# Performance work log

Hardware: AMD Instinct MI355X
Metric: run time of the kernel (lower is better)

Reference implementation:

```python
import jax, jax.numpy as jnp
import numpy as np

DN = ('NCH', 'OIH', 'NCH')

def conv1d(x, w, b, pad):
    y = jax.lax.conv_general_dilated(x, w, (1,), [(pad, pad)], dimension_numbers=DN)
    return y if b is None else y + b[None, :, None]

def bn_eval(x, g, b, m, v, eps):
    s = g * jax.lax.rsqrt(v + eps)
    return x * s[None, :, None] + (b - m * s)[None, :, None]

def swish(x):
    return x * jax.nn.sigmoid(x)

def setup_inputs() -> dict:
    key = jax.random.key(0)
    ks = jax.random.split(key, 8)
    B, T, P = 16, 8192, 32
    inp = {
        'x': jax.random.normal(ks[0], (B, 1, T), jnp.float32),
        'conv_w': jax.random.normal(ks[1], (512, 1, 9), jnp.float32) * 0.1,
        'bn_g': jnp.ones((512,), jnp.float32),
        'bn_b': jnp.zeros((512,), jnp.float32),
        'bn_m': jnp.zeros((512,), jnp.float32),
        'bn_v': jnp.ones((512,), jnp.float32),
        'p1_w': jax.random.normal(ks[2], (P, 2, 31), jnp.float32) * 0.1,
        'p1_b': jnp.zeros((P,), jnp.float32),
        'pbn1_g': jnp.ones((P,), jnp.float32),
        'pbn1_b': jnp.zeros((P,), jnp.float32),
        'pbn1_m': jnp.zeros((P,), jnp.float32),
        'pbn1_v': jnp.ones((P,), jnp.float32),
        'p2_w': jax.random.normal(ks[3], (P, P, 15), jnp.float32) * 0.05,
        'p2_b': jnp.zeros((P,), jnp.float32),
        'pbn2_g': jnp.ones((P,), jnp.float32),
        'pbn2_b': jnp.zeros((P,), jnp.float32),
        'pbn2_m': jnp.zeros((P,), jnp.float32),
        'pbn2_v': jnp.ones((P,), jnp.float32),
        'p3_w': jax.random.normal(ks[4], (2, P, 15), jnp.float32) * 0.001,  # source scales last conv weight by 0.01
        'p3_b': jnp.full((2,), -np.log(2.0), jnp.float32),                 # source sets bias to -log(2)
        'norm_mean': jnp.ones((1,), jnp.float32),                           # eval-mode renorm buffer
    }
    return inp

def reference(x, conv_w, bn_g, bn_b, bn_m, bn_v,
              p1_w, p1_b, pbn1_g, pbn1_b, pbn1_m, pbn1_v,
              p2_w, p2_b, pbn2_g, pbn2_b, pbn2_m, pbn2_v,
              p3_w, p3_b, norm_mean):
    B, _, T = x.shape
    # main conv -> BN(eps=1e-3) -> GLU(dim=1); dropout is identity in eval
    h = conv1d(x, conv_w, None, 9 // 2)                 # [B, 512, T]
    h = bn_eval(h, bn_g, bn_b, bn_m, bn_v, 1e-3)
    a, g = jnp.split(h, 2, axis=1)
    features = a * jax.nn.sigmoid(g)                    # [B, 256, T]
    # predictor on cat([x, x*x])
    j = conv1d(jnp.concatenate([x, x * x], axis=1), p1_w, p1_b, 15)
    j = swish(bn_eval(j, pbn1_g, pbn1_b, pbn1_m, pbn1_v, 1e-5))
    j = conv1d(j, p2_w, p2_b, 7)
    j = swish(bn_eval(j, pbn2_g, pbn2_b, pbn2_m, pbn2_v, 1e-5))
    j = conv1d(j, p3_w, p3_b, 7)                        # [B, 2, T]
    weights = jax.nn.sigmoid(j[:, 0, :])                # [B, T]
    moves = jax.nn.sigmoid(j[:, 1, :])
    bmoves = moves
    moves = moves * norm_mean[0]                        # eval: renorm = norm_mean buffer
    # CIF-style dynamic pooling (row_pool), vectorized over batch
    feats = jnp.transpose(features, (0, 2, 1))          # [B, T, C]
    fw = feats * weights[..., None]
    poses = jnp.cumsum(jax.lax.stop_gradient(moves), axis=1)  # moves.detach() in source
    floors = jnp.floor(poses)
    w1 = 1.0 - (poses - floors)
    w2 = poses - floors
    fl = floors.astype(jnp.int32)
    ce = fl + 1
    Lmax = T + 2  # static bound: poses <= T so ceil index <= T+1
    C = fw.shape[2]
    def pool(fw_i, fl_i, ce_i, w1_i, w2_i):
        out = jnp.zeros((Lmax, C), fw_i.dtype)
        out = out.at[fl_i].add(w1_i[:, None] * fw_i)
        out = out.at[ce_i].add(w2_i[:, None] * fw_i)
        return out
    x_evs = jax.vmap(pool)(fw, fl, ce, w1, w2)          # [B, Lmax, C]
    lens = fl[:, -1] + 2                                 # int(ceils[-1]) + 1
    x_evs = jnp.transpose(x_evs, (0, 2, 1))             # [B, C, Lmax]
    pad = 3 - (Lmax % 3)
    x_evs = jnp.pad(x_evs, ((0, 0), (0, 0), (0, pad)))
    return x_evs, lens, bmoves, weights
```

## Files before the change

kernel.cpp:

```cpp
#include <hip/hip_runtime.h>
#include <math.h>

static constexpr int TT = 8192;
static constexpr int LFULL = 8196;

static constexpr size_t XE_OFF   = 0;
static constexpr size_t LENS_OFF = (size_t)16*256*LFULL;
static constexpr size_t BM_OFF   = LENS_OFF + 16;
static constexpr size_t WT_OFF   = BM_OFF + (size_t)16*TT;

static constexpr size_t U_OFF     = 0;
static constexpr size_t V_OFF     = U_OFF + (size_t)16*32*TT;
static constexpr size_t MOVES_OFF = V_OFF + (size_t)16*32*TT;
static constexpr size_t POSES_OFF = MOVES_OFF + (size_t)16*TT;
static constexpr size_t C1_OFF    = POSES_OFF + (size_t)16*TT;
static constexpr size_t C2_OFF    = C1_OFF + (size_t)16*TT;

__device__ __forceinline__ float sig_(float z) { return 1.0f / (1.0f + __expf(-z)); }

__global__ __launch_bounds__(256) void k_conv1(
    const float* __restrict__ x,
    const float* __restrict__ p1w, const float* __restrict__ p1b,
    const float* __restrict__ g1, const float* __restrict__ b1,
    const float* __restrict__ m1, const float* __restrict__ v1,
    float* __restrict__ u)
{
    __shared__ float xin[2 * 320];
    __shared__ float w1t[2 * 992];
    const int tid = threadIdx.x;
    const int b = blockIdx.y;
    const int t0 = blockIdx.x * 256;

    for (int idx = tid; idx < 640; idx += 256) {
        int ci = idx / 320, xl = idx - ci * 320;
        int id = t0 - 15 + xl;
        float val = 0.f;
        if (xl < 286 && id >= 0 && id < TT) val = x[b * TT + id];
        xin[idx] = ci ? val * val : val;
    }
    for (int idx = tid; idx < 1984; idx += 256) {
        int c = idx / 62; int r = idx - c * 62; int ci = r / 31; int k = r - ci * 31;
        w1t[ci * 992 + c * 31 + k] = p1w[idx];
    }
    __syncthreads();

    const int tg = tid >> 5, c = tid & 31;
    float acc[32];
    const float bias = p1b[c];
#pragma unroll
    for (int i = 0; i < 32; ++i) acc[i] = bias;

    for (int h = 0; h < 4; ++h) {
        for (int ci = 0; ci < 2; ++ci) {
            float win[40];
            const float4* wp = (const float4*)(&xin[ci * 320 + tg * 32 + h * 8]);
#pragma unroll
            for (int r = 0; r < 10; ++r) {
                float4 q = wp[r];
                win[4*r] = q.x; win[4*r+1] = q.y; win[4*r+2] = q.z; win[4*r+3] = q.w;
            }
#pragma unroll
            for (int k = 0; k < 31; ++k) {
                float w = w1t[ci * 992 + c * 31 + k];
#pragma unroll
                for (int i = 0; i < 8; ++i) acc[h*8+i] = fmaf(w, win[i + k], acc[h*8+i]);
            }
        }
    }
    const float s = g1[c] * rsqrtf(v1[c] + 1e-5f);
    const float sh = b1[c] - m1[c] * s;
    float* up = &u[((size_t)(b * 32 + c)) * TT + t0 + tg * 32];
#pragma unroll
    for (int i = 0; i < 8; ++i) {
        float z0 = fmaf(acc[4*i+0], s, sh);
        float z1 = fmaf(acc[4*i+1], s, sh);
        float z2 = fmaf(acc[4*i+2], s, sh);
        float z3 = fmaf(acc[4*i+3], s, sh);
        ((float4*)up)[i] = make_float4(z0 * sig_(z0), z1 * sig_(z1), z2 * sig_(z2), z3 * sig_(z3));
    }
}

__global__ __launch_bounds__(256) void k_conv2(
    const float* __restrict__ u,
    const float* __restrict__ p2w, const float* __restrict__ p2b,
    const float* __restrict__ g2, const float* __restrict__ b2,
    const float* __restrict__ m2, const float* __restrict__ v2,
    float* __restrict__ vout)
{
    __shared__ float uld[32 * 144];
    __shared__ float w2t[32 * 240];
    const int tid = threadIdx.x;
    const int b = blockIdx.y;
    const int t0 = blockIdx.x * 128;
    const int ch = blockIdx.z;

    for (int idx = tid; idx < 32 * 144; idx += 256) {
        int ci = idx / 144, tl = idx - ci * 144;
        int tg = t0 - 7 + tl;
        float val = 0.f;
        if (tl < 142 && tg >= 0 && tg < TT) val = u[((size_t)(b * 32 + ci)) * TT + tg];
        uld[idx] = val;
    }
    for (int idx = tid; idx < 32 * 240; idx += 256) {
        int ci = idx / 240; int r = idx - ci * 240; int cl = r / 15; int k = r - cl * 15;
        w2t[idx] = p2w[(ch * 16 + cl) * 480 + ci * 15 + k];
    }
    __syncthreads();

    const int tg = tid >> 4, cl = tid & 15;
    const int c = ch * 16 + cl;
    float acc[8];
    const float bias = p2b[c];
#pragma unroll
    for (int i = 0; i < 8; ++i) acc[i] = bias;

    for (int ci = 0; ci < 32; ++ci) {
        float win[24];
        const float4* wp = (const float4*)(&uld[ci * 144 + tg * 8]);
#pragma unroll
        for (int r = 0; r < 6; ++r) {
            float4 q = wp[r];
            win[4*r] = q.x; win[4*r+1] = q.y; win[4*r+2] = q.z; win[4*r+3] = q.w;
        }
#pragma unroll
        for (int k = 0; k < 15; ++k) {
            float w = w2t[ci * 240 + cl * 15 + k];
#pragma unroll
            for (int i = 0; i < 8; ++i) acc[i] = fmaf(w, win[i + k], acc[i]);
        }
    }
    const float s = g2[c] * rsqrtf(v2[c] + 1e-5f);
    const float sh = b2[c] - m2[c] * s;
    float o[8];
#pragma unroll
    for (int i = 0; i < 8; ++i) { float z = fmaf(acc[i], s, sh); o[i] = z * sig_(z); }
    float* vp = &vout[((size_t)(b * 32 + c)) * TT + t0 + tg * 8];
    ((float4*)vp)[0] = make_float4(o[0], o[1], o[2], o[3]);
    ((float4*)vp)[1] = make_float4(o[4], o[5], o[6], o[7]);
}

__global__ __launch_bounds__(256) void k_conv3(
    const float* __restrict__ vin,
    const float* __restrict__ p3w, const float* __restrict__ p3b,
    const float* __restrict__ nm,
    float* __restrict__ outw, float* __restrict__ outbm, float* __restrict__ moves)
{
    __shared__ float vld[32 * 272];
    const int tid = threadIdx.x;
    const int b = blockIdx.y;
    const int t0 = blockIdx.x * 256;

    for (int idx = tid; idx < 32 * 272; idx += 256) {
        int ci = idx / 272, tl = idx - ci * 272;
        int tg = t0 - 7 + tl;
        float val = 0.f;
        if (tl < 270 && tg >= 0 && tg < TT) val = vin[((size_t)(b * 32 + ci)) * TT + tg];
        vld[idx] = val;
    }
    __syncthreads();

    float a0 = p3b[0], a1 = p3b[1];
    for (int ci = 0; ci < 32; ++ci) {
        float win[15];
#pragma unroll
        for (int k = 0; k < 15; ++k) win[k] = vld[ci * 272 + tid + k];
#pragma unroll
        for (int k = 0; k < 15; ++k) {
            a0 = fmaf(p3w[ci * 15 + k], win[k], a0);
            a1 = fmaf(p3w[480 + ci * 15 + k], win[k], a1);
        }
    }
    const int t = t0 + tid;
    const float wt = sig_(a0);
    const float bm = sig_(a1);
    outw[b * TT + t] = wt;
    outbm[b * TT + t] = bm;
    moves[b * TT + t] = bm * nm[0];
}

__global__ __launch_bounds__(1024) void k_scan(
    const float* __restrict__ moves, const float* __restrict__ wts,
    float* __restrict__ poses, float* __restrict__ coef1, float* __restrict__ coef2,
    float* __restrict__ lens)
{
    __shared__ float wsum[16];
    const int tid = threadIdx.x;
    const int b = blockIdx.x;
    const int lane = tid & 63, wv = tid >> 6;
    float carry = 0.f;

    const float4* mv4 = (const float4*)&moves[b * TT];
    const float4* wt4 = (const float4*)&wts[b * TT];
    float4* po4 = (float4*)&poses[b * TT];
    float4* c14 = (float4*)&coef1[b * TT];
    float4* c24 = (float4*)&coef2[b * TT];

    for (int chunk = 0; chunk < 2; ++chunk) {
        const int idx = chunk * 1024 + tid;
        float4 m = mv4[idx];
        const float s = m.x + m.y + m.z + m.w;
        float v = s;
#pragma unroll
        for (int off = 1; off < 64; off <<= 1) {
            float n = __shfl_up(v, off, 64);
            if (lane >= off) v += n;
        }
        if (lane == 63) wsum[wv] = v;
        __syncthreads();
        float pre = carry;
        for (int w = 0; w < wv; ++w) pre += wsum[w];
        float tot = 0.f;
#pragma unroll
        for (int w = 0; w < 16; ++w) tot += wsum[w];
        const float base = pre + (v - s);
        const float p0 = base + m.x;
        const float p1 = p0 + m.y;
        const float p2 = p1 + m.z;
        const float p3 = p2 + m.w;
        po4[idx] = make_float4(p0, p1, p2, p3);
        const float4 w4 = wt4[idx];
        const float fr0 = p0 - floorf(p0), fr1 = p1 - floorf(p1);
        const float fr2 = p2 - floorf(p2), fr3 = p3 - floorf(p3);
        c14[idx] = make_float4((1.f - fr0) * w4.x, (1.f - fr1) * w4.y,
                               (1.f - fr2) * w4.z, (1.f - fr3) * w4.w);
        c24[idx] = make_float4(fr0 * w4.x, fr1 * w4.y, fr2 * w4.z, fr3 * w4.w);
        if (chunk == 1 && tid == 1023) lens[b] = floorf(p3) + 2.0f;
        carry += tot;
        __syncthreads();
    }
}

static constexpr int LTILE = 32;
static constexpr int CHK = 256;

__global__ __launch_bounds__(256) void k_pool(
    const float* __restrict__ x,
    const float* __restrict__ cw,
    const float* __restrict__ bng, const float* __restrict__ bnb,
    const float* __restrict__ bnm, const float* __restrict__ bnv,
    const float* __restrict__ poses, const float* __restrict__ coef1, const float* __restrict__ coef2,
    float* __restrict__ xevs)
{
    __shared__ float out_lds[256 * 33];
    __shared__ float4 xl4[68];
    __shared__ float4 c1l4[CHK / 4], c2l4[CHK / 4];
    __shared__ int lbs[LTILE + 2];
    float* xl = (float*)xl4;
    float* c1l = (float*)c1l4;
    float* c2l = (float*)c2l4;

    const int tid = threadIdx.x;
    const int b = blockIdx.y;
    const int l0 = blockIdx.x * LTILE;
    const int LTa = min(LTILE, LFULL - l0);

    if (tid < LTa + 2) {
        const float lf = (float)(l0 - 1 + tid);
        int lo = 0, hi = TT;
        const float* pp = &poses[b * TT];
        while (lo < hi) { int mid = (lo + hi) >> 1; if (pp[mid] >= lf) hi = mid; else lo = mid + 1; }
        lbs[tid] = lo;
    }
    __syncthreads();

    const int t_lo = lbs[0];
    const int t_hi = lbs[LTa + 1];
    const size_t rowbase = (size_t)b * 256 * LFULL + l0;

    if (t_lo >= t_hi) {
        const float4 z = make_float4(0.f, 0.f, 0.f, 0.f);
#pragma unroll
        for (int it = 0; it < 8; ++it) {
            int idx4 = it * 256 + tid;
            int cc = idx4 >> 3, q = (idx4 & 7) << 2;
            if (l0 + q < LFULL)
                *(float4*)(&xevs[rowbase + (size_t)cc * LFULL + q]) = z;
        }
        return;
    }

    {
        float4 z = make_float4(0.f, 0.f, 0.f, 0.f);
        float4* oz = (float4*)out_lds;
        for (int idx = tid; idx < (256 * 33) / 4; idx += 256) oz[idx] = z;
    }

    const int c = tid;
    float wa[9], wg[9];
#pragma unroll
    for (int k = 0; k < 9; ++k) { wa[k] = cw[c * 9 + k]; wg[k] = cw[(c + 256) * 9 + k]; }
    const float sa = bng[c] * rsqrtf(bnv[c] + 1e-3f);
    const float sha = bnb[c] - bnm[c] * sa;
    const float sg = bng[c + 256] * rsqrtf(bnv[c + 256] + 1e-3f);
    const float shg = bnb[c + 256] - bnm[c + 256] * sg;

    const float* xg = &x[b * TT];
    const float* c1g = &coef1[b * TT];
    const float* c2g = &coef2[b * TT];

    float accA = 0.f, accB = 0.f;
    int j = 0;
    int nb = lbs[1];

    for (int cs = t_lo; cs < t_hi; cs += CHK) {
        const int ce = min(cs + CHK, t_hi);
        const int len = ce - cs;
        __syncthreads();
        for (int idx = tid; idx < len + 12; idx += 256) {
            int id = cs - 4 + idx;
            xl[idx] = (id >= 0 && id < TT) ? xg[id] : 0.f;
        }
        if (tid < len) { c1l[tid] = c1g[cs + tid]; c2l[tid] = c2g[cs + tid]; }
        __syncthreads();

        const int len4 = len >> 2;
        for (int g = 0; g < len4; ++g) {
            float4 A = xl4[g], Bq = xl4[g + 1], Cq = xl4[g + 2];
            float w[12] = {A.x, A.y, A.z, A.w, Bq.x, Bq.y, Bq.z, Bq.w, Cq.x, Cq.y, Cq.z, Cq.w};
            float f[4];
#pragma unroll
            for (int i = 0; i < 4; ++i) {
                float s0 = 0.f, s1 = 0.f;
#pragma unroll
                for (int k = 0; k < 9; ++k) { s0 = fmaf(wa[k], w[i + k], s0); s1 = fmaf(wg[k], w[i + k], s1); }
                const float av = fmaf(s0, sa, sha);
                const float gv = fmaf(s1, sg, shg);
                f[i] = av * sig_(gv);
            }
            float4 c1v = c1l4[g], c2v = c2l4[g];
            const float c1a[4] = {c1v.x, c1v.y, c1v.z, c1v.w};
            const float c2a[4] = {c2v.x, c2v.y, c2v.z, c2v.w};
            const int tb = cs + (g << 2);
#pragma unroll
            for (int i = 0; i < 4; ++i) {
                const int t = tb + i;
                while (t >= nb) {
                    int li = j - 1;
                    if (li >= 0 && li < LTa) out_lds[c * 33 + li] = accA;
                    accA = accB; accB = 0.f;
                    ++j;
                    nb = lbs[j + 1];
                }
                accA = fmaf(c1a[i], f[i], accA);
                accB = fmaf(c2a[i], f[i], accB);
            }
        }
        for (int t = cs + (len4 << 2); t < ce; ++t) {
            const int il = t - cs;
            float s0 = 0.f, s1 = 0.f;
#pragma unroll
            for (int k = 0; k < 9; ++k) { float xv = xl[il + k]; s0 = fmaf(wa[k], xv, s0); s1 = fmaf(wg[k], xv, s1); }
            const float av = fmaf(s0, sa, sha);
            const float gv = fmaf(s1, sg, shg);
            const float f0 = av * sig_(gv);
            while (t >= nb) {
                int li = j - 1;
                if (li >= 0 && li < LTa) out_lds[c * 33 + li] = accA;
                accA = accB; accB = 0.f;
                ++j;
                nb = lbs[j + 1];
            }
            accA = fmaf(c1l[il], f0, accA);
            accB = fmaf(c2l[il], f0, accB);
        }
    }
    {
        int li = j - 1;
        if (li >= 0 && li < LTa) out_lds[c * 33 + li] = accA;
    }
    __syncthreads();

#pragma unroll
    for (int it = 0; it < 8; ++it) {
        int idx4 = it * 256 + tid;
        int cc = idx4 >> 3, q = (idx4 & 7) << 2;
        if (l0 + q < LFULL) {
            float4 o;
            o.x = out_lds[cc * 33 + q + 0];
            o.y = out_lds[cc * 33 + q + 1];
            o.z = out_lds[cc * 33 + q + 2];
            o.w = out_lds[cc * 33 + q + 3];
            *(float4*)(&xevs[rowbase + (size_t)cc * LFULL + q]) = o;
        }
    }
}

extern "C" void kernel_launch(void* const* d_in, const int* in_sizes, int n_in,
                              void* d_out, int out_size, void* d_ws, size_t ws_size,
                              hipStream_t stream) {
    (void)in_sizes; (void)n_in; (void)out_size; (void)ws_size;
    const float* x      = (const float*)d_in[0];
    const float* conv_w = (const float*)d_in[1];
    const float* bn_g   = (const float*)d_in[2];
    const float* bn_b   = (const float*)d_in[3];
    const float* bn_m   = (const float*)d_in[4];
    const float* bn_v   = (const float*)d_in[5];
    const float* p1_w   = (const float*)d_in[6];
    const float* p1_b   = (const float*)d_in[7];
    const float* pbn1_g = (const float*)d_in[8];
    const float* pbn1_b = (const float*)d_in[9];
    const float* pbn1_m = (const float*)d_in[10];
    const float* pbn1_v = (const float*)d_in[11];
    const float* p2_w   = (const float*)d_in[12];
    const float* p2_b   = (const float*)d_in[13];
    const float* pbn2_g = (const float*)d_in[14];
    const float* pbn2_b = (const float*)d_in[15];
    const float* pbn2_m = (const float*)d_in[16];
    const float* pbn2_v = (const float*)d_in[17];
    const float* p3_w   = (const float*)d_in[18];
    const float* p3_b   = (const float*)d_in[19];
    const float* nm     = (const float*)d_in[20];

    float* out = (float*)d_out;
    float* ws  = (float*)d_ws;
    float* u     = ws + U_OFF;
    float* v     = ws + V_OFF;
    float* moves = ws + MOVES_OFF;
    float* poses = ws + POSES_OFF;
    float* coef1 = ws + C1_OFF;
    float* coef2 = ws + C2_OFF;
    float* xevs  = out + XE_OFF;
    float* lens  = out + LENS_OFF;
    float* bmv   = out + BM_OFF;
    float* wts   = out + WT_OFF;

    k_conv1<<<dim3(32, 16), 256, 0, stream>>>(x, p1_w, p1_b, pbn1_g, pbn1_b, pbn1_m, pbn1_v, u);
    k_conv2<<<dim3(64, 16, 2), 256, 0, stream>>>(u, p2_w, p2_b, pbn2_g, pbn2_b, pbn2_m, pbn2_v, v);
    k_conv3<<<dim3(32, 16), 256, 0, stream>>>(v, p3_w, p3_b, nm, wts, bmv, moves);
    k_scan<<<16, 1024, 0, stream>>>(moves, wts, poses, coef1, coef2, lens);
    k_pool<<<dim3(257, 16), 256, 0, stream>>>(x, conv_w, bn_g, bn_b, bn_m, bn_v, poses, coef1, coef2, xevs);
}
```

Baseline: 365.7 us.

## Emit segment boundaries from scan and halve pool tile size

The scan kernel now writes, for each output slot, the first input index whose cumulative position reaches it, so the pool kernel reads its boundaries directly instead of binary-searching the poses array. The poses buffer is dropped and the boundary array reuses the start of the workspace already consumed by the earlier conv stages. The pool tile shrinks from 32 to 16 output slots with a smaller chunk, doubling the grid to improve occupancy and load balance, at the cost of recomputing more halo convolution work per block. The boundary fill loop in the scan is serial per thread, so a thread whose positions cross many slot boundaries does extra work.

```diff
diff --git a/kernel.cpp b/kernel.cpp
--- a/kernel.cpp
+++ b/kernel.cpp
@@ -3,6 +3,7 @@
 
 static constexpr int TT = 8192;
 static constexpr int LFULL = 8196;
+static constexpr int BSTRIDE = LFULL + 2;
 
 static constexpr size_t XE_OFF   = 0;
 static constexpr size_t LENS_OFF = (size_t)16*256*LFULL;
@@ -12,9 +13,9 @@
 static constexpr size_t U_OFF     = 0;
 static constexpr size_t V_OFF     = U_OFF + (size_t)16*32*TT;
 static constexpr size_t MOVES_OFF = V_OFF + (size_t)16*32*TT;
-static constexpr size_t POSES_OFF = MOVES_OFF + (size_t)16*TT;
-static constexpr size_t C1_OFF    = POSES_OFF + (size_t)16*TT;
+static constexpr size_t C1_OFF    = MOVES_OFF + (size_t)16*TT;
 static constexpr size_t C2_OFF    = C1_OFF + (size_t)16*TT;
+static constexpr size_t BND_OFF   = U_OFF;
 
 __device__ __forceinline__ float sig_(float z) { return 1.0f / (1.0f + __expf(-z)); }
 
@@ -180,8 +181,8 @@
 
 __global__ __launch_bounds__(1024) void k_scan(
     const float* __restrict__ moves, const float* __restrict__ wts,
-    float* __restrict__ poses, float* __restrict__ coef1, float* __restrict__ coef2,
-    float* __restrict__ lens)
+    float* __restrict__ coef1, float* __restrict__ coef2,
+    int* __restrict__ bnd, float* __restrict__ lens)
 {
     __shared__ float wsum[16];
     const int tid = threadIdx.x;
@@ -189,9 +190,13 @@
     const int lane = tid & 63, wv = tid >> 6;
     float carry = 0.f;
 
+    int* bb = &bnd[b * BSTRIDE];
+    for (int i = tid; i < BSTRIDE; i += 1024) bb[i] = TT;
+    if (tid == 0) { bb[0] = 0; bb[1] = 0; }
+    __syncthreads();
+
     const float4* mv4 = (const float4*)&moves[b * TT];
     const float4* wt4 = (const float4*)&wts[b * TT];
-    float4* po4 = (float4*)&poses[b * TT];
     float4* c14 = (float4*)&coef1[b * TT];
     float4* c24 = (float4*)&coef2[b * TT];
 
@@ -217,32 +222,46 @@
         const float p1 = p0 + m.y;
         const float p2 = p1 + m.z;
         const float p3 = p2 + m.w;
-        po4[idx] = make_float4(p0, p1, p2, p3);
         const float4 w4 = wt4[idx];
         const float fr0 = p0 - floorf(p0), fr1 = p1 - floorf(p1);
         const float fr2 = p2 - floorf(p2), fr3 = p3 - floorf(p3);
         c14[idx] = make_float4((1.f - fr0) * w4.x, (1.f - fr1) * w4.y,
                                (1.f - fr2) * w4.z, (1.f - fr3) * w4.w);
         c24[idx] = make_float4(fr0 * w4.x, fr1 * w4.y, fr2 * w4.z, fr3 * w4.w);
+        {
+            int lf = (int)floorf(base) + 1;
+            const int lfe = (int)floorf(p3);
+            const int tbase = idx << 2;
+            for (; lf <= lfe; ++lf) {
+                const float lff = (float)lf;
+                int t = tbase;
+                if (p0 >= lff) { }
+                else if (p1 >= lff) t += 1;
+                else if (p2 >= lff) t += 2;
+                else t += 3;
+                if (lf + 1 < BSTRIDE) bb[lf + 1] = t;
+            }
+        }
         if (chunk == 1 && tid == 1023) lens[b] = floorf(p3) + 2.0f;
         carry += tot;
         __syncthreads();
     }
 }
 
-static constexpr int LTILE = 32;
-static constexpr int CHK = 256;
+static constexpr int LTILE = 16;
+static constexpr int CHK = 128;
 
 __global__ __launch_bounds__(256) void k_pool(
     const float* __restrict__ x,
     const float* __restrict__ cw,
     const float* __restrict__ bng, const float* __restrict__ bnb,
     const float* __restrict__ bnm, const float* __restrict__ bnv,
-    const float* __restrict__ poses, const float* __restrict__ coef1, const float* __restrict__ coef2,
+    const float* __restrict__ coef1, const float* __restrict__ coef2,
+    const int* __restrict__ bnd,
     float* __restrict__ xevs)
 {
-    __shared__ float out_lds[256 * 33];
-    __shared__ float4 xl4[68];
+    __shared__ float out_lds[256 * 17];
+    __shared__ float4 xl4[36];
     __shared__ float4 c1l4[CHK / 4], c2l4[CHK / 4];
     __shared__ int lbs[LTILE + 2];
     float* xl = (float*)xl4;
@@ -254,13 +273,7 @@
     const int l0 = blockIdx.x * LTILE;
     const int LTa = min(LTILE, LFULL - l0);
 
-    if (tid < LTa + 2) {
-        const float lf = (float)(l0 - 1 + tid);
-        int lo = 0, hi = TT;
-        const float* pp = &poses[b * TT];
-        while (lo < hi) { int mid = (lo + hi) >> 1; if (pp[mid] >= lf) hi = mid; else lo = mid + 1; }
-        lbs[tid] = lo;
-    }
+    if (tid < LTa + 2) lbs[tid] = bnd[b * BSTRIDE + l0 + tid];
     __syncthreads();
 
     const int t_lo = lbs[0];
@@ -270,19 +283,18 @@
     if (t_lo >= t_hi) {
         const float4 z = make_float4(0.f, 0.f, 0.f, 0.f);
 #pragma unroll
-        for (int it = 0; it < 8; ++it) {
+        for (int it = 0; it < 4; ++it) {
             int idx4 = it * 256 + tid;
-            int cc = idx4 >> 3, q = (idx4 & 7) << 2;
-            if (l0 + q < LFULL)
+            int cc = idx4 >> 2, q = (idx4 & 3) << 2;
+            if (q < LTa)
                 *(float4*)(&xevs[rowbase + (size_t)cc * LFULL + q]) = z;
         }
         return;
     }
 
     {
-        float4 z = make_float4(0.f, 0.f, 0.f, 0.f);
-        float4* oz = (float4*)out_lds;
-        for (int idx = tid; idx < (256 * 33) / 4; idx += 256) oz[idx] = z;
+#pragma unroll
+        for (int li = 0; li < 17; ++li) out_lds[tid * 17 + li] = 0.f;
     }
 
     const int c = tid;
@@ -336,7 +348,7 @@
                 const int t = tb + i;
                 while (t >= nb) {
                     int li = j - 1;
-                    if (li >= 0 && li < LTa) out_lds[c * 33 + li] = accA;
+                    if (li >= 0 && li < LTa) out_lds[c * 17 + li] = accA;
                     accA = accB; accB = 0.f;
                     ++j;
                     nb = lbs[j + 1];
@@ -355,7 +367,7 @@
             const float f0 = av * sig_(gv);
             while (t >= nb) {
                 int li = j - 1;
-                if (li >= 0 && li < LTa) out_lds[c * 33 + li] = accA;
+                if (li >= 0 && li < LTa) out_lds[c * 17 + li] = accA;
                 accA = accB; accB = 0.f;
                 ++j;
                 nb = lbs[j + 1];
@@ -366,20 +378,20 @@
     }
     {
         int li = j - 1;
-        if (li >= 0 && li < LTa) out_lds[c * 33 + li] = accA;
-    }
-    __syncthreads();
-
-#pragma unroll
-    for (int it = 0; it < 8; ++it) {
+        if (li >= 0 && li < LTa) out_lds[c * 17 + li] = accA;
+    }
+    __syncthreads();
+
+#pragma unroll
+    for (int it = 0; it < 4; ++it) {
         int idx4 = it * 256 + tid;
-        int cc = idx4 >> 3, q = (idx4 & 7) << 2;
-        if (l0 + q < LFULL) {
+        int cc = idx4 >> 2, q = (idx4 & 3) << 2;
+        if (q < LTa) {
             float4 o;
-            o.x = out_lds[cc * 33 + q + 0];
-            o.y = out_lds[cc * 33 + q + 1];
-            o.z = out_lds[cc * 33 + q + 2];
-            o.w = out_lds[cc * 33 + q + 3];
+            o.x = out_lds[cc * 17 + q + 0];
+            o.y = out_lds[cc * 17 + q + 1];
+            o.z = out_lds[cc * 17 + q + 2];
+            o.w = out_lds[cc * 17 + q + 3];
             *(float4*)(&xevs[rowbase + (size_t)cc * LFULL + q]) = o;
         }
     }
@@ -416,9 +428,9 @@
     float* u     = ws + U_OFF;
     float* v     = ws + V_OFF;
     float* moves = ws + MOVES_OFF;
-    float* poses = ws + POSES_OFF;
     float* coef1 = ws + C1_OFF;
     float* coef2 = ws + C2_OFF;
+    int*   bnd   = (int*)(ws + BND_OFF);
     float* xevs  = out + XE_OFF;
     float* lens  = out + LENS_OFF;
     float* bmv   = out + BM_OFF;
@@ -427,6 +439,7 @@
     k_conv1<<<dim3(32, 16), 256, 0, stream>>>(x, p1_w, p1_b, pbn1_g, pbn1_b, pbn1_m, pbn1_v, u);
     k_conv2<<<dim3(64, 16, 2), 256, 0, stream>>>(u, p2_w, p2_b, pbn2_g, pbn2_b, pbn2_m, pbn2_v, v);
     k_conv3<<<dim3(32, 16), 256, 0, stream>>>(v, p3_w, p3_b, nm, wts, bmv, moves);
-    k_scan<<<16, 1024, 0, stream>>>(moves, wts, poses, coef1, coef2, lens);
-    k_pool<<<dim3(257, 16), 256, 0, stream>>>(x, conv_w, bn_g, bn_b, bn_m, bn_v, poses, coef1, coef2, xevs);
-}
+    k_scan<<<16, 1024, 0, stream>>>(moves, wts, coef1, coef2, bnd, lens);
+    k_pool<<<dim3((LFULL + LTILE - 1) / LTILE, 16), 256, 0, stream>>>(
+        x, conv_w, bn_g, bn_b, bn_m, bn_v, coef1, coef2, bnd, xevs);
+}
```

Result: slower. 376.8 us (+3.0%).
